# Kernel optimization log

Hardware: AMD Instinct MI355X
Metric: run time of the kernel (lower is better)

Reference implementation:

```python
import jax, jax.numpy as jnp
import numpy as np
import math

DIM = 512
HEADS = 8
DH = DIM // HEADS
B, C, H, W = 2, 512, 48, 48


def setup_inputs() -> dict:
    key = jax.random.key(0)
    k1, k2, k3, k4 = jax.random.split(key, 4)
    x = jax.random.normal(k1, (B, C, H, W), dtype=jnp.float32)
    # torch Linear weights: [out_features, in_features]
    w_qkv = jax.random.normal(k2, (3 * DIM, DIM), dtype=jnp.float32) * (DIM ** -0.5)
    w_out = jax.random.normal(k3, (DIM, DIM), dtype=jnp.float32) * (DIM ** -0.5)
    b_out = jax.random.normal(k4, (DIM,), dtype=jnp.float32) * 0.01
    wavelength = jnp.asarray(0.1, dtype=jnp.float32)
    return {"x": x, "w_qkv": w_qkv, "w_out": w_out, "b_out": b_out, "wavelength": wavelength}


def reference(x, w_qkv, w_out, b_out, wavelength):
    b, c, h, w = x.shape
    n = h * w
    scale = DH ** -0.5

    x_flat = x.reshape(b, c, n).transpose(0, 2, 1)  # [B, N, C]
    qkv = jnp.einsum('bnc,dc->bnd', x_flat, w_qkv)   # [B, N, 3*DIM]
    q, k, v = jnp.split(qkv, 3, axis=-1)

    def to_heads(t):
        return t.reshape(b, n, HEADS, DH).transpose(0, 2, 1, 3)  # [B, h, N, dh]

    q, k, v = to_heads(q), to_heads(k), to_heads(v)

    dots = jnp.einsum('bhid,bhjd->bhij', q, k) * scale  # [B, h, N, N]

    # Fresnel interference bias over spatial positions
    yy, xx = jnp.meshgrid(jnp.arange(h), jnp.arange(w), indexing='ij')
    positions = jnp.stack([yy, xx], axis=-1).astype(jnp.float32).reshape(-1, 2)  # [N, 2]
    pos_diff = positions[None, :, :] - positions[:, None, :]  # [N, N, 2]
    distances = jnp.sqrt(jnp.sum(pos_diff ** 2, axis=-1) + 1e-8)  # [N, N]
    phase = 2.0 * math.pi * distances / (jnp.abs(wavelength) * h + 1e-6)
    interference = jnp.cos(phase)

    dots = dots + interference[None, None, :, :] * 0.1
    attn = jax.nn.softmax(dots, axis=-1)
    out = jnp.einsum('bhij,bhjd->bhid', attn, v)  # [B, h, N, dh]
    out = out.transpose(0, 2, 1, 3).reshape(b, n, HEADS * DH)  # [B, N, DIM]
    out = jnp.einsum('bnd,od->bno', out, w_out) + b_out
    return out.transpose(0, 2, 1).reshape(b, c, h, w)
```

## Files before the change

### kernel.cpp

```cpp
#include <hip/hip_runtime.h>
#include <math.h>

#define BB 2
#define CC 512
#define NN 2304
#define NH 8
#define DD 512
#define D3 1536
#define WIDTH 48
#define C1 0.18033688f

typedef _Float16 h8 __attribute__((ext_vector_type(8)));
typedef _Float16 h4 __attribute__((ext_vector_type(4)));
typedef _Float16 h2 __attribute__((ext_vector_type(2)));
typedef float f4 __attribute__((ext_vector_type(4)));

__device__ __forceinline__ void gload16(const void* g, void* s) {
  __builtin_amdgcn_global_load_lds(
      (const __attribute__((address_space(1))) unsigned int*)g,
      (__attribute__((address_space(3))) unsigned int*)s, 16, 0, 0);
}

__global__ __launch_bounds__(128) void btf_k(const float* __restrict__ wavp,
                                             _Float16* __restrict__ btf)
{
  const int t = threadIdx.x;
  const int qbk = blockIdx.x, ktk = blockIdx.y;
  const int w = t >> 6, quad = (t >> 4) & 3, l15 = t & 15;
  const float pc = 6.283185307179586f / (fabsf(wavp[0]) * (float)WIDTH + 1e-6f);
  _Float16* o = btf + (((size_t)qbk * 36 + ktk) * 128 + t) * 32;
#pragma unroll
  for (int g = 0; g < 4; ++g) {
    h8 v;
#pragma unroll
    for (int e = 0; e < 8; ++e) {
      const int j = g * 8 + e;
      const int nt = j >> 4, mt = (j >> 2) & 3, r = j & 3;
      const int q = qbk * 64 + w * 32 + nt * 16 + l15;
      const int k = ktk * 64 + mt * 16 + quad * 4 + r;
      const float dy = (float)(q / WIDTH) - (float)(k / WIDTH);
      const float dx = (float)(q % WIDTH) - (float)(k % WIDTH);
      const float dist = sqrtf(dy * dy + dx * dx + 1e-8f);
      v[e] = (_Float16)(0.1f * __cosf(dist * pc) * 1.44269504f);
    }
    *(h8*)(o + g * 8) = v;
  }
}

__global__ __launch_bounds__(256) void tx_k(const float* __restrict__ x,
                                            _Float16* __restrict__ xt)
{
  __shared__ float Ls[32][33];
  const int t = threadIdx.x;
  const int n0 = blockIdx.x * 32, c0 = blockIdx.y * 32, b = blockIdx.z;
#pragma unroll
  for (int p = 0; p < 4; ++p) {
    const int cl = (t >> 5) + p * 8, nl = t & 31;
    Ls[cl][nl] = x[((size_t)b * CC + c0 + cl) * NN + n0 + nl];
  }
  __syncthreads();
#pragma unroll
  for (int p = 0; p < 2; ++p) {
    const int nl = (t >> 4) + p * 16, cl = (t & 15) * 2;
    h2 v = {(_Float16)Ls[cl][nl], (_Float16)Ls[cl + 1][nl]};
    *(h2*)(xt + ((size_t)b * NN + n0 + nl) * CC + c0 + cl) = v;
  }
}

__global__ __launch_bounds__(256) void convw_k(const float* __restrict__ wq,
                                               const float* __restrict__ wo,
                                               _Float16* __restrict__ wqh,
                                               _Float16* __restrict__ woh)
{
  const int idx = blockIdx.x * 256 + threadIdx.x;
  const int NQ = (D3 * CC) / 4;
  if (idx < NQ) {
    float4 v = *(const float4*)(wq + (size_t)idx * 4);
    h4 o = {(_Float16)v.x, (_Float16)v.y, (_Float16)v.z, (_Float16)v.w};
    *(h4*)(wqh + (size_t)idx * 4) = o;
  } else {
    const int j = idx - NQ;
    float4 v = *(const float4*)(wo + (size_t)j * 4);
    h4 o = {(_Float16)v.x, (_Float16)v.y, (_Float16)v.z, (_Float16)v.w};
    *(h4*)(woh + (size_t)j * 4) = o;
  }
}

__global__ __launch_bounds__(256) void qkv_gemm_k(
    const _Float16* __restrict__ xt, const _Float16* __restrict__ wqh,
    _Float16* __restrict__ qb, _Float16* __restrict__ kb,
    _Float16* __restrict__ vb)
{
  __shared__ _Float16 Xs[128][32];
  __shared__ _Float16 Ws[128][32];
  const int t = threadIdx.x;
  const int lane = t & 63, w = t >> 6;
  const int l15 = lane & 15, quad = lane >> 4;
  const int wm = w & 1, wn = w >> 1;
  const int n0 = blockIdx.x * 128;
  const int d0 = blockIdx.y * 128;
  const int b  = blockIdx.z;
  const bool isv = (d0 >= 2 * DD);
  const _Float16* xb = xt + (size_t)b * NN * CC;

  const int srow = lane >> 2, scol = (lane & 3) * 8;

  f4 acc[4][4];
#pragma unroll
  for (int mt = 0; mt < 4; ++mt)
#pragma unroll
    for (int nt = 0; nt < 4; ++nt) acc[mt][nt] = (f4)(0.f);

  for (int c0 = 0; c0 < CC; c0 += 32) {
#pragma unroll
    for (int r = 0; r < 2; ++r) {
      const int ci = w + r * 4;
      const int row = ci * 16 + srow;
      gload16(xb + (size_t)(n0 + row) * CC + c0 + scol, &Xs[0][0] + ci * 512);
      gload16(wqh + (size_t)(d0 + row) * CC + c0 + scol, &Ws[0][0] + ci * 512);
    }
    __syncthreads();

    h8 wfr[4], xfr[4];
#pragma unroll
    for (int mt = 0; mt < 4; ++mt)
      wfr[mt] = *(const h8*)&Ws[wm * 64 + mt * 16 + l15][quad * 8];
#pragma unroll
    for (int nt = 0; nt < 4; ++nt)
      xfr[nt] = *(const h8*)&Xs[wn * 64 + nt * 16 + l15][quad * 8];

    if (!isv) {
#pragma unroll
      for (int mt = 0; mt < 4; ++mt)
#pragma unroll
        for (int nt = 0; nt < 4; ++nt)
          acc[mt][nt] = __builtin_amdgcn_mfma_f32_16x16x32_f16(
              wfr[mt], xfr[nt], acc[mt][nt], 0, 0, 0);
    } else {
#pragma unroll
      for (int mt = 0; mt < 4; ++mt)
#pragma unroll
        for (int nt = 0; nt < 4; ++nt)
          acc[mt][nt] = __builtin_amdgcn_mfma_f32_16x16x32_f16(
              xfr[nt], wfr[mt], acc[mt][nt], 0, 0, 0);
    }
    __syncthreads();
  }

  if (!isv) {
    const int which = d0 >> 9;
    _Float16* buf = which == 0 ? qb : kb;
    const int h = ((d0 & 511) >> 6) + wm;
#pragma unroll
    for (int mt = 0; mt < 4; ++mt) {
      const int dh = mt * 16 + quad * 4;
#pragma unroll
      for (int nt = 0; nt < 4; ++nt) {
        const int token = n0 + wn * 64 + nt * 16 + l15;
        h4 o = {(_Float16)acc[mt][nt][0], (_Float16)acc[mt][nt][1],
                (_Float16)acc[mt][nt][2], (_Float16)acc[mt][nt][3]};
        *(h4*)(buf + (((size_t)b * NH + h) * NN + token) * 64 + dh) = o;
      }
    }
  } else {
    const int h = ((d0 - 2 * DD) >> 6) + wm;
#pragma unroll
    for (int mt = 0; mt < 4; ++mt) {
      const int dh = mt * 16 + l15;
#pragma unroll
      for (int nt = 0; nt < 4; ++nt) {
        const int token = n0 + wn * 64 + nt * 16 + quad * 4;
        h4 o = {(_Float16)acc[mt][nt][0], (_Float16)acc[mt][nt][1],
                (_Float16)acc[mt][nt][2], (_Float16)acc[mt][nt][3]};
        *(h4*)(vb + (((size_t)b * NH + h) * 64 + dh) * NN + token) = o;
      }
    }
  }
}

__global__ __launch_bounds__(128, 3) void attn_k(
    const _Float16* __restrict__ qb, const _Float16* __restrict__ kb,
    const _Float16* __restrict__ vb, const _Float16* __restrict__ btf,
    _Float16* __restrict__ op, float* __restrict__ lp)
{
  __shared__ _Float16 Ks[64][72];
  __shared__ _Float16 Vs[64][72];
  __shared__ _Float16 Ps[64][72];

  const int t    = threadIdx.x;
  const int lane = t & 63;
  const int w    = t >> 6;
  const int l15  = lane & 15;
  const int quad = lane >> 4;
  const int qtile = blockIdx.x >> 1;
  const int khalf = blockIdx.x & 1;
  const int n0 = qtile * 64;
  const int h  = blockIdx.y;
  const int b  = blockIdx.z;
  const size_t base = ((size_t)b * NH + h) * NN * 64;
  const _Float16* qp = qb + base;
  const _Float16* kp = kb + base;
  const _Float16* vp = vb + base;

  h8 qf[2][2];
#pragma unroll
  for (int nt = 0; nt < 2; ++nt)
#pragma unroll
    for (int ks = 0; ks < 2; ++ks)
      qf[nt][ks] = *(const h8*)(qp + (size_t)(n0 + w * 32 + nt * 16 + l15) * 64 +
                                ks * 32 + quad * 8);

  f4 oc[4][2];
#pragma unroll
  for (int mt = 0; mt < 4; ++mt)
#pragma unroll
    for (int nt = 0; nt < 2; ++nt) oc[mt][nt] = (f4)(0.f);
  float lacc[2][4] = {};

  const _Float16* bp = btf + (((size_t)qtile * 36 + khalf * 18) * 128 + t) * 32;

  for (int kt = 0; kt < 18; ++kt) {
    const int k0 = (khalf * 18 + kt) * 64;
    h8 kr[4], vr[4], bfr[4];
#pragma unroll
    for (int r = 0; r < 4; ++r) {
      const int c = t + r * 128;
      const int row = c >> 3, off = (c & 7) * 8;
      kr[r] = *(const h8*)(kp + (size_t)(k0 + row) * 64 + off);
      vr[r] = *(const h8*)(vp + (size_t)row * NN + k0 + off);
      bfr[r] = *(const h8*)(bp + r * 8);
    }
    bp += 128 * 32;
    __syncthreads();
#pragma unroll
    for (int r = 0; r < 4; ++r) {
      const int c = t + r * 128;
      const int row = c >> 3, off = (c & 7) * 8;
      *(h8*)&Ks[row][off] = kr[r];
      *(h8*)&Vs[row][off] = vr[r];
    }
    __syncthreads();

    f4 st[4][2];
#pragma unroll
    for (int mt = 0; mt < 4; ++mt)
#pragma unroll
      for (int nt = 0; nt < 2; ++nt) st[mt][nt] = (f4)(0.f);
#pragma unroll
    for (int ks = 0; ks < 2; ++ks) {
#pragma unroll
      for (int mt = 0; mt < 4; ++mt) {
        h8 kf = *(const h8*)&Ks[mt * 16 + l15][ks * 32 + quad * 8];
#pragma unroll
        for (int nt = 0; nt < 2; ++nt)
          st[mt][nt] = __builtin_amdgcn_mfma_f32_16x16x32_f16(
              kf, qf[nt][ks], st[mt][nt], 0, 0, 0);
      }
    }

#pragma unroll
    for (int nt = 0; nt < 2; ++nt) {
      const int q = w * 32 + nt * 16 + l15;
#pragma unroll
      for (int mt = 0; mt < 4; ++mt) {
        h4 pk;
#pragma unroll
        for (int r = 0; r < 4; ++r) {
          const int j = nt * 16 + mt * 4 + r;
          const float bias = (float)bfr[j >> 3][j & 7];
          const float p = __builtin_exp2f(st[mt][nt][r] * C1 + bias);
          lacc[nt][r] += p;
          pk[r] = (_Float16)p;
        }
        *(h4*)&Ps[q][mt * 16 + quad * 4] = pk;
      }
    }

#pragma unroll
    for (int ks = 0; ks < 2; ++ks) {
      h8 pf[2];
#pragma unroll
      for (int nt = 0; nt < 2; ++nt)
        pf[nt] = *(const h8*)&Ps[w * 32 + nt * 16 + l15][ks * 32 + quad * 8];
#pragma unroll
      for (int mt = 0; mt < 4; ++mt) {
        h8 vf = *(const h8*)&Vs[mt * 16 + l15][ks * 32 + quad * 8];
#pragma unroll
        for (int nt = 0; nt < 2; ++nt)
          oc[mt][nt] = __builtin_amdgcn_mfma_f32_16x16x32_f16(
              vf, pf[nt], oc[mt][nt], 0, 0, 0);
      }
    }
  }

#pragma unroll
  for (int nt = 0; nt < 2; ++nt) {
    float l = lacc[nt][0] + lacc[nt][1] + lacc[nt][2] + lacc[nt][3];
    l += __shfl_xor(l, 16);
    l += __shfl_xor(l, 32);
    const float inv = 1.f / l;
    const int qi = n0 + w * 32 + nt * 16 + l15;
    _Float16* od = op + (size_t)khalf * BB * NN * DD +
                   ((size_t)b * NN + qi) * DD + h * 64;
#pragma unroll
    for (int mt = 0; mt < 4; ++mt) {
      const int dh = mt * 16 + quad * 4;
      h4 o = {(_Float16)(oc[mt][nt][0] * inv), (_Float16)(oc[mt][nt][1] * inv),
              (_Float16)(oc[mt][nt][2] * inv), (_Float16)(oc[mt][nt][3] * inv)};
      *(h4*)(od + dh) = o;
    }
    if (quad == 0)
      lp[(size_t)khalf * BB * NH * NN + ((size_t)b * NH + h) * NN + qi] = l;
  }
}

__global__ __launch_bounds__(256) void comb_k(
    const _Float16* __restrict__ op, const float* __restrict__ lp,
    _Float16* __restrict__ ho)
{
  const int idx = blockIdx.x * 256 + threadIdx.x;
  const int d8 = idx & 63;
  const int bn = idx >> 6;
  const int n = bn % NN, b = bn / NN;
  const int h = d8 >> 3;
  const float l0 = lp[((size_t)b * NH + h) * NN + n];
  const float l1 = lp[(size_t)BB * NH * NN + ((size_t)b * NH + h) * NN + n];
  const float inv = 1.f / (l0 + l1);
  const float w0 = l0 * inv, w1 = l1 * inv;
  h8 o0 = *(const h8*)(op + (size_t)bn * DD + d8 * 8);
  h8 o1 = *(const h8*)(op + (size_t)BB * NN * DD + (size_t)bn * DD + d8 * 8);
  h8 r;
#pragma unroll
  for (int i = 0; i < 8; ++i)
    r[i] = (_Float16)((float)o0[i] * w0 + (float)o1[i] * w1);
  *(h8*)(ho + (size_t)bn * DD + d8 * 8) = r;
}

__global__ __launch_bounds__(64) void out_gemm_k(
    const _Float16* __restrict__ ho, const _Float16* __restrict__ woh,
    const float* __restrict__ bias, float* __restrict__ out)
{
  __shared__ _Float16 Hs[64][32];
  __shared__ _Float16 Ws2[64][32];
  const int t = threadIdx.x;
  const int l15 = t & 15, quad = t >> 4;
  const int n0 = blockIdx.x * 64;
  const int o0 = blockIdx.y * 64;
  const int b  = blockIdx.z;
  const int srow = t >> 2, scol = (t & 3) * 8;

  f4 acc[4][4];
#pragma unroll
  for (int mt = 0; mt < 4; ++mt)
#pragma unroll
    for (int nt = 0; nt < 4; ++nt) acc[mt][nt] = (f4)(0.f);

  for (int c0 = 0; c0 < DD; c0 += 32) {
#pragma unroll
    for (int ci = 0; ci < 4; ++ci) {
      const int row = ci * 16 + srow;
      gload16(ho + ((size_t)b * NN + n0 + row) * DD + c0 + scol,
              &Hs[0][0] + ci * 512);
      gload16(woh + (size_t)(o0 + row) * DD + c0 + scol,
              &Ws2[0][0] + ci * 512);
    }
    __syncthreads();
    h8 hf[4], wf[4];
#pragma unroll
    for (int mt = 0; mt < 4; ++mt)
      hf[mt] = *(const h8*)&Hs[mt * 16 + l15][quad * 8];
#pragma unroll
    for (int nt = 0; nt < 4; ++nt)
      wf[nt] = *(const h8*)&Ws2[nt * 16 + l15][quad * 8];
#pragma unroll
    for (int mt = 0; mt < 4; ++mt)
#pragma unroll
      for (int nt = 0; nt < 4; ++nt)
        acc[mt][nt] = __builtin_amdgcn_mfma_f32_16x16x32_f16(
            hf[mt], wf[nt], acc[mt][nt], 0, 0, 0);
    __syncthreads();
  }

#pragma unroll
  for (int nt = 0; nt < 4; ++nt) {
    const int o = o0 + nt * 16 + l15;
    const float bv = bias[o];
#pragma unroll
    for (int mt = 0; mt < 4; ++mt) {
      const int token = n0 + mt * 16 + quad * 4;
      float4 v = {acc[mt][nt][0] + bv, acc[mt][nt][1] + bv,
                  acc[mt][nt][2] + bv, acc[mt][nt][3] + bv};
      *(float4*)(out + ((size_t)b * DD + o) * NN + token) = v;
    }
  }
}

extern "C" void kernel_launch(void* const* d_in, const int* in_sizes, int n_in,
                              void* d_out, int out_size, void* d_ws, size_t ws_size,
                              hipStream_t stream)
{
  (void)in_sizes; (void)n_in; (void)out_size; (void)ws_size;
  const float* x     = (const float*)d_in[0];
  const float* w_qkv = (const float*)d_in[1];
  const float* w_out = (const float*)d_in[2];
  const float* b_out = (const float*)d_in[3];
  const float* wav   = (const float*)d_in[4];
  float* out = (float*)d_out;

  const size_t SZ  = (size_t)BB * NH * NN * 64;
  const size_t BTF = (size_t)36 * 36 * 128 * 32;

  _Float16* qb  = (_Float16*)d_ws;
  _Float16* kb  = qb + SZ;
  _Float16* vb  = kb + SZ;
  _Float16* btf = vb + SZ;
  _Float16* op  = btf + BTF;
  float*    lpf = (float*)(op + 2 * SZ);
  _Float16* woh = (_Float16*)(lpf + 2 * (size_t)BB * NH * NN);
  _Float16* ho  = btf;
  _Float16* xt  = op;
  _Float16* wqh = op + SZ;

  btf_k     <<<dim3(36, 36), 128, 0, stream>>>(wav, btf);
  tx_k      <<<dim3(NN / 32, CC / 32, BB), 256, 0, stream>>>(x, xt);
  convw_k   <<<dim3((D3 * CC + DD * DD) / 1024), 256, 0, stream>>>(w_qkv, w_out, wqh, woh);
  qkv_gemm_k<<<dim3(NN / 128, D3 / 128, BB), 256, 0, stream>>>(xt, wqh, qb, kb, vb);
  attn_k    <<<dim3(NN / 64 * 2, NH, BB), 128, 0, stream>>>(qb, kb, vb, btf, op, lpf);
  comb_k    <<<dim3((BB * NN * 64) / 256), 256, 0, stream>>>(op, lpf, ho);
  out_gemm_k<<<dim3(NN / 64, DD / 64, BB), 64, 0, stream>>>(ho, woh, b_out, out);
}
```

Before: 169.3 us.

## Load MFMA operands directly from global memory, dropping shared-memory staging

```diff
diff --git a/kernel.cpp b/kernel.cpp
--- a/kernel.cpp
+++ b/kernel.cpp
@@ -14,12 +14,6 @@
 typedef _Float16 h4 __attribute__((ext_vector_type(4)));
 typedef _Float16 h2 __attribute__((ext_vector_type(2)));
 typedef float f4 __attribute__((ext_vector_type(4)));
-
-__device__ __forceinline__ void gload16(const void* g, void* s) {
-  __builtin_amdgcn_global_load_lds(
-      (const __attribute__((address_space(1))) unsigned int*)g,
-      (__attribute__((address_space(3))) unsigned int*)s, 16, 0, 0);
-}
 
 __global__ __launch_bounds__(128) void btf_k(const float* __restrict__ wavp,
                                              _Float16* __restrict__ btf)
@@ -91,8 +85,6 @@
     _Float16* __restrict__ qb, _Float16* __restrict__ kb,
     _Float16* __restrict__ vb)
 {
-  __shared__ _Float16 Xs[128][32];
-  __shared__ _Float16 Ws[128][32];
   const int t = threadIdx.x;
   const int lane = t & 63, w = t >> 6;
   const int l15 = lane & 15, quad = lane >> 4;
@@ -102,8 +94,8 @@
   const int b  = blockIdx.z;
   const bool isv = (d0 >= 2 * DD);
   const _Float16* xb = xt + (size_t)b * NN * CC;
-
-  const int srow = lane >> 2, scol = (lane & 3) * 8;
+  const _Float16* wp = wqh + (size_t)(d0 + wm * 64 + l15) * CC + quad * 8;
+  const _Float16* xp = xb + (size_t)(n0 + wn * 64 + l15) * CC + quad * 8;
 
   f4 acc[4][4];
 #pragma unroll
@@ -111,24 +103,15 @@
 #pragma unroll
     for (int nt = 0; nt < 4; ++nt) acc[mt][nt] = (f4)(0.f);
 
+#pragma unroll 2
   for (int c0 = 0; c0 < CC; c0 += 32) {
-#pragma unroll
-    for (int r = 0; r < 2; ++r) {
-      const int ci = w + r * 4;
-      const int row = ci * 16 + srow;
-      gload16(xb + (size_t)(n0 + row) * CC + c0 + scol, &Xs[0][0] + ci * 512);
-      gload16(wqh + (size_t)(d0 + row) * CC + c0 + scol, &Ws[0][0] + ci * 512);
-    }
-    __syncthreads();
-
     h8 wfr[4], xfr[4];
 #pragma unroll
     for (int mt = 0; mt < 4; ++mt)
-      wfr[mt] = *(const h8*)&Ws[wm * 64 + mt * 16 + l15][quad * 8];
+      wfr[mt] = *(const h8*)(wp + (size_t)mt * 16 * CC + c0);
 #pragma unroll
     for (int nt = 0; nt < 4; ++nt)
-      xfr[nt] = *(const h8*)&Xs[wn * 64 + nt * 16 + l15][quad * 8];
-
+      xfr[nt] = *(const h8*)(xp + (size_t)nt * 16 * CC + c0);
     if (!isv) {
 #pragma unroll
       for (int mt = 0; mt < 4; ++mt)
@@ -144,7 +127,6 @@
           acc[mt][nt] = __builtin_amdgcn_mfma_f32_16x16x32_f16(
               xfr[nt], wfr[mt], acc[mt][nt], 0, 0, 0);
     }
-    __syncthreads();
   }
 
   if (!isv) {
@@ -183,20 +165,14 @@
     const _Float16* __restrict__ vb, const _Float16* __restrict__ btf,
     _Float16* __restrict__ op, float* __restrict__ lp)
 {
-  __shared__ _Float16 Ks[64][72];
-  __shared__ _Float16 Vs[64][72];
-  __shared__ _Float16 Ps[64][72];
-
-  const int t    = threadIdx.x;
-  const int lane = t & 63;
-  const int w    = t >> 6;
-  const int l15  = lane & 15;
-  const int quad = lane >> 4;
-  const int qtile = blockIdx.x >> 1;
-  const int khalf = blockIdx.x & 1;
-  const int n0 = qtile * 64;
-  const int h  = blockIdx.y;
-  const int b  = blockIdx.z;
+  __shared__ _Float16 Ps[2][32][72];
+  const int t = threadIdx.x;
+  const int lane = t & 63, w = t >> 6;
+  const int l15 = lane & 15, quad = lane >> 4;
+  const int qt = blockIdx.x >> 1;
+  const int s  = blockIdx.x & 1;
+  const int h = blockIdx.y, b = blockIdx.z;
+  const int n0 = qt * 64 + w * 32;
   const size_t base = ((size_t)b * NH + h) * NN * 64;
   const _Float16* qp = qb + base;
   const _Float16* kp = kb + base;
@@ -207,7 +183,7 @@
   for (int nt = 0; nt < 2; ++nt)
 #pragma unroll
     for (int ks = 0; ks < 2; ++ks)
-      qf[nt][ks] = *(const h8*)(qp + (size_t)(n0 + w * 32 + nt * 16 + l15) * 64 +
+      qf[nt][ks] = *(const h8*)(qp + (size_t)(n0 + nt * 16 + l15) * 64 +
                                 ks * 32 + quad * 8);
 
   f4 oc[4][2];
@@ -217,29 +193,21 @@
     for (int nt = 0; nt < 2; ++nt) oc[mt][nt] = (f4)(0.f);
   float lacc[2][4] = {};
 
-  const _Float16* bp = btf + (((size_t)qtile * 36 + khalf * 18) * 128 + t) * 32;
+  const _Float16* bp = btf + (((size_t)qt * 36 + s * 18) * 128 + t) * 32;
 
   for (int kt = 0; kt < 18; ++kt) {
-    const int k0 = (khalf * 18 + kt) * 64;
-    h8 kr[4], vr[4], bfr[4];
-#pragma unroll
-    for (int r = 0; r < 4; ++r) {
-      const int c = t + r * 128;
-      const int row = c >> 3, off = (c & 7) * 8;
-      kr[r] = *(const h8*)(kp + (size_t)(k0 + row) * 64 + off);
-      vr[r] = *(const h8*)(vp + (size_t)row * NN + k0 + off);
-      bfr[r] = *(const h8*)(bp + r * 8);
-    }
+    const int k0 = (s * 18 + kt) * 64;
+    h8 bfr[4];
+#pragma unroll
+    for (int r = 0; r < 4; ++r) bfr[r] = *(const h8*)(bp + r * 8);
     bp += 128 * 32;
-    __syncthreads();
-#pragma unroll
-    for (int r = 0; r < 4; ++r) {
-      const int c = t + r * 128;
-      const int row = c >> 3, off = (c & 7) * 8;
-      *(h8*)&Ks[row][off] = kr[r];
-      *(h8*)&Vs[row][off] = vr[r];
-    }
-    __syncthreads();
+    h8 kf[2][4];
+#pragma unroll
+    for (int ks = 0; ks < 2; ++ks)
+#pragma unroll
+      for (int mt = 0; mt < 4; ++mt)
+        kf[ks][mt] = *(const h8*)(kp + (size_t)(k0 + mt * 16 + l15) * 64 +
+                                  ks * 32 + quad * 8);
 
     f4 st[4][2];
 #pragma unroll
@@ -247,20 +215,25 @@
 #pragma unroll
       for (int nt = 0; nt < 2; ++nt) st[mt][nt] = (f4)(0.f);
 #pragma unroll
-    for (int ks = 0; ks < 2; ++ks) {
-#pragma unroll
-      for (int mt = 0; mt < 4; ++mt) {
-        h8 kf = *(const h8*)&Ks[mt * 16 + l15][ks * 32 + quad * 8];
+    for (int ks = 0; ks < 2; ++ks)
+#pragma unroll
+      for (int mt = 0; mt < 4; ++mt)
 #pragma unroll
         for (int nt = 0; nt < 2; ++nt)
           st[mt][nt] = __builtin_amdgcn_mfma_f32_16x16x32_f16(
-              kf, qf[nt][ks], st[mt][nt], 0, 0, 0);
-      }
-    }
+              kf[ks][mt], qf[nt][ks], st[mt][nt], 0, 0, 0);
+
+    h8 vf[2][4];
+#pragma unroll
+    for (int ks = 0; ks < 2; ++ks)
+#pragma unroll
+      for (int mt = 0; mt < 4; ++mt)
+        vf[ks][mt] = *(const h8*)(vp + (size_t)(mt * 16 + l15) * NN + k0 +
+                                  ks * 32 + quad * 8);
 
 #pragma unroll
     for (int nt = 0; nt < 2; ++nt) {
-      const int q = w * 32 + nt * 16 + l15;
+      const int q = nt * 16 + l15;
 #pragma unroll
       for (int mt = 0; mt < 4; ++mt) {
         h4 pk;
@@ -272,7 +245,7 @@
           lacc[nt][r] += p;
           pk[r] = (_Float16)p;
         }
-        *(h4*)&Ps[q][mt * 16 + quad * 4] = pk;
+        *(h4*)&Ps[w][q][mt * 16 + quad * 4] = pk;
       }
     }
 
@@ -281,15 +254,13 @@
       h8 pf[2];
 #pragma unroll
       for (int nt = 0; nt < 2; ++nt)
-        pf[nt] = *(const h8*)&Ps[w * 32 + nt * 16 + l15][ks * 32 + quad * 8];
-#pragma unroll
-      for (int mt = 0; mt < 4; ++mt) {
-        h8 vf = *(const h8*)&Vs[mt * 16 + l15][ks * 32 + quad * 8];
+        pf[nt] = *(const h8*)&Ps[w][nt * 16 + l15][ks * 32 + quad * 8];
+#pragma unroll
+      for (int mt = 0; mt < 4; ++mt)
 #pragma unroll
         for (int nt = 0; nt < 2; ++nt)
           oc[mt][nt] = __builtin_amdgcn_mfma_f32_16x16x32_f16(
-              vf, pf[nt], oc[mt][nt], 0, 0, 0);
-      }
+              vf[ks][mt], pf[nt], oc[mt][nt], 0, 0, 0);
     }
   }
 
@@ -299,8 +270,8 @@
     l += __shfl_xor(l, 16);
     l += __shfl_xor(l, 32);
     const float inv = 1.f / l;
-    const int qi = n0 + w * 32 + nt * 16 + l15;
-    _Float16* od = op + (size_t)khalf * BB * NN * DD +
+    const int qi = n0 + nt * 16 + l15;
+    _Float16* od = op + (size_t)s * BB * NN * DD +
                    ((size_t)b * NN + qi) * DD + h * 64;
 #pragma unroll
     for (int mt = 0; mt < 4; ++mt) {
@@ -310,7 +281,7 @@
       *(h4*)(od + dh) = o;
     }
     if (quad == 0)
-      lp[(size_t)khalf * BB * NH * NN + ((size_t)b * NH + h) * NN + qi] = l;
+      lp[(size_t)s * BB * NH * NN + ((size_t)b * NH + h) * NN + qi] = l;
   }
 }
 
@@ -340,14 +311,13 @@
     const _Float16* __restrict__ ho, const _Float16* __restrict__ woh,
     const float* __restrict__ bias, float* __restrict__ out)
 {
-  __shared__ _Float16 Hs[64][32];
-  __shared__ _Float16 Ws2[64][32];
   const int t = threadIdx.x;
   const int l15 = t & 15, quad = t >> 4;
   const int n0 = blockIdx.x * 64;
   const int o0 = blockIdx.y * 64;
   const int b  = blockIdx.z;
-  const int srow = t >> 2, scol = (t & 3) * 8;
+  const _Float16* hp = ho + ((size_t)b * NN + n0 + l15) * DD + quad * 8;
+  const _Float16* wp = woh + (size_t)(o0 + l15) * DD + quad * 8;
 
   f4 acc[4][4];
 #pragma unroll
@@ -355,30 +325,21 @@
 #pragma unroll
     for (int nt = 0; nt < 4; ++nt) acc[mt][nt] = (f4)(0.f);
 
+#pragma unroll 2
   for (int c0 = 0; c0 < DD; c0 += 32) {
-#pragma unroll
-    for (int ci = 0; ci < 4; ++ci) {
-      const int row = ci * 16 + srow;
-      gload16(ho + ((size_t)b * NN + n0 + row) * DD + c0 + scol,
-              &Hs[0][0] + ci * 512);
-      gload16(woh + (size_t)(o0 + row) * DD + c0 + scol,
-              &Ws2[0][0] + ci * 512);
-    }
-    __syncthreads();
     h8 hf[4], wf[4];
 #pragma unroll
     for (int mt = 0; mt < 4; ++mt)
-      hf[mt] = *(const h8*)&Hs[mt * 16 + l15][quad * 8];
+      hf[mt] = *(const h8*)(hp + (size_t)mt * 16 * DD + c0);
 #pragma unroll
     for (int nt = 0; nt < 4; ++nt)
-      wf[nt] = *(const h8*)&Ws2[nt * 16 + l15][quad * 8];
+      wf[nt] = *(const h8*)(wp + (size_t)nt * 16 * DD + c0);
 #pragma unroll
     for (int mt = 0; mt < 4; ++mt)
 #pragma unroll
       for (int nt = 0; nt < 4; ++nt)
         acc[mt][nt] = __builtin_amdgcn_mfma_f32_16x16x32_f16(
             hf[mt], wf[nt], acc[mt][nt], 0, 0, 0);
-    __syncthreads();
   }
 
 #pragma unroll
```

New measurement: 231.0 us. 36.5% more time.

## Double-buffer GEMM tiles and prefetch next K/V tile in attention

Applied to the files above, without the earlier changes.

```diff
diff --git a/kernel.cpp b/kernel.cpp
--- a/kernel.cpp
+++ b/kernel.cpp
@@ -86,24 +86,21 @@
   }
 }
 
-__global__ __launch_bounds__(256) void qkv_gemm_k(
+__global__ __launch_bounds__(64) void qkv_gemm_k(
     const _Float16* __restrict__ xt, const _Float16* __restrict__ wqh,
     _Float16* __restrict__ qb, _Float16* __restrict__ kb,
     _Float16* __restrict__ vb)
 {
-  __shared__ _Float16 Xs[128][32];
-  __shared__ _Float16 Ws[128][32];
+  __shared__ _Float16 Xs[2][64][32];
+  __shared__ _Float16 Ws[2][64][32];
   const int t = threadIdx.x;
-  const int lane = t & 63, w = t >> 6;
-  const int l15 = lane & 15, quad = lane >> 4;
-  const int wm = w & 1, wn = w >> 1;
-  const int n0 = blockIdx.x * 128;
-  const int d0 = blockIdx.y * 128;
+  const int l15 = t & 15, quad = t >> 4;
+  const int n0 = blockIdx.x * 64;
+  const int d0 = blockIdx.y * 64;
   const int b  = blockIdx.z;
   const bool isv = (d0 >= 2 * DD);
   const _Float16* xb = xt + (size_t)b * NN * CC;
-
-  const int srow = lane >> 2, scol = (lane & 3) * 8;
+  const int srow = t >> 2, scol = (t & 3) * 8;
 
   f4 acc[4][4];
 #pragma unroll
@@ -111,24 +108,29 @@
 #pragma unroll
     for (int nt = 0; nt < 4; ++nt) acc[mt][nt] = (f4)(0.f);
 
-  for (int c0 = 0; c0 < CC; c0 += 32) {
-#pragma unroll
-    for (int r = 0; r < 2; ++r) {
-      const int ci = w + r * 4;
+  auto stage = [&](int bf, int c0) {
+#pragma unroll
+    for (int ci = 0; ci < 4; ++ci) {
       const int row = ci * 16 + srow;
-      gload16(xb + (size_t)(n0 + row) * CC + c0 + scol, &Xs[0][0] + ci * 512);
-      gload16(wqh + (size_t)(d0 + row) * CC + c0 + scol, &Ws[0][0] + ci * 512);
-    }
+      gload16(xb + (size_t)(n0 + row) * CC + c0 + scol,
+              &Xs[bf][0][0] + ci * 512);
+      gload16(wqh + (size_t)(d0 + row) * CC + c0 + scol,
+              &Ws[bf][0][0] + ci * 512);
+    }
+  };
+
+  stage(0, 0);
+  for (int i = 0; i < 16; ++i) {
+    const int cur = i & 1;
     __syncthreads();
-
+    if (i < 15) stage(cur ^ 1, (i + 1) * 32);
     h8 wfr[4], xfr[4];
 #pragma unroll
     for (int mt = 0; mt < 4; ++mt)
-      wfr[mt] = *(const h8*)&Ws[wm * 64 + mt * 16 + l15][quad * 8];
+      wfr[mt] = *(const h8*)&Ws[cur][mt * 16 + l15][quad * 8];
 #pragma unroll
     for (int nt = 0; nt < 4; ++nt)
-      xfr[nt] = *(const h8*)&Xs[wn * 64 + nt * 16 + l15][quad * 8];
-
+      xfr[nt] = *(const h8*)&Xs[cur][nt * 16 + l15][quad * 8];
     if (!isv) {
 #pragma unroll
       for (int mt = 0; mt < 4; ++mt)
@@ -144,32 +146,31 @@
           acc[mt][nt] = __builtin_amdgcn_mfma_f32_16x16x32_f16(
               xfr[nt], wfr[mt], acc[mt][nt], 0, 0, 0);
     }
-    __syncthreads();
   }
 
   if (!isv) {
     const int which = d0 >> 9;
     _Float16* buf = which == 0 ? qb : kb;
-    const int h = ((d0 & 511) >> 6) + wm;
+    const int h = (d0 & 511) >> 6;
 #pragma unroll
     for (int mt = 0; mt < 4; ++mt) {
       const int dh = mt * 16 + quad * 4;
 #pragma unroll
       for (int nt = 0; nt < 4; ++nt) {
-        const int token = n0 + wn * 64 + nt * 16 + l15;
+        const int token = n0 + nt * 16 + l15;
         h4 o = {(_Float16)acc[mt][nt][0], (_Float16)acc[mt][nt][1],
                 (_Float16)acc[mt][nt][2], (_Float16)acc[mt][nt][3]};
         *(h4*)(buf + (((size_t)b * NH + h) * NN + token) * 64 + dh) = o;
       }
     }
   } else {
-    const int h = ((d0 - 2 * DD) >> 6) + wm;
+    const int h = (d0 - 2 * DD) >> 6;
 #pragma unroll
     for (int mt = 0; mt < 4; ++mt) {
       const int dh = mt * 16 + l15;
 #pragma unroll
       for (int nt = 0; nt < 4; ++nt) {
-        const int token = n0 + wn * 64 + nt * 16 + quad * 4;
+        const int token = n0 + nt * 16 + quad * 4;
         h4 o = {(_Float16)acc[mt][nt][0], (_Float16)acc[mt][nt][1],
                 (_Float16)acc[mt][nt][2], (_Float16)acc[mt][nt][3]};
         *(h4*)(vb + (((size_t)b * NH + h) * 64 + dh) * NN + token) = o;
@@ -185,18 +186,17 @@
 {
   __shared__ _Float16 Ks[64][72];
   __shared__ _Float16 Vs[64][72];
-  __shared__ _Float16 Ps[64][72];
+  __shared__ _Float16 Ps[2][32][72];
 
   const int t    = threadIdx.x;
   const int lane = t & 63;
   const int w    = t >> 6;
   const int l15  = lane & 15;
   const int quad = lane >> 4;
-  const int qtile = blockIdx.x >> 1;
-  const int khalf = blockIdx.x & 1;
-  const int n0 = qtile * 64;
-  const int h  = blockIdx.y;
-  const int b  = blockIdx.z;
+  const int qt = blockIdx.x >> 1;
+  const int s  = blockIdx.x & 1;
+  const int h = blockIdx.y, b = blockIdx.z;
+  const int n0 = qt * 64;
   const size_t base = ((size_t)b * NH + h) * NN * 64;
   const _Float16* qp = qb + base;
   const _Float16* kp = kb + base;
@@ -217,29 +217,45 @@
     for (int nt = 0; nt < 2; ++nt) oc[mt][nt] = (f4)(0.f);
   float lacc[2][4] = {};
 
-  const _Float16* bp = btf + (((size_t)qtile * 36 + khalf * 18) * 128 + t) * 32;
+  const int srow = t >> 3, soff = (t & 7) * 8;
+  const _Float16* bp = btf + (((size_t)qt * 36 + s * 18) * 128 + t) * 32;
+
+  h8 kr[4], vr[4], br[4];
+  {
+    const int k0 = s * 18 * 64;
+#pragma unroll
+    for (int r = 0; r < 4; ++r) {
+      const int row = srow + r * 16;
+      kr[r] = *(const h8*)(kp + (size_t)(k0 + row) * 64 + soff);
+      vr[r] = *(const h8*)(vp + (size_t)row * NN + k0 + soff);
+      br[r] = *(const h8*)(bp + r * 8);
+    }
+  }
 
   for (int kt = 0; kt < 18; ++kt) {
-    const int k0 = (khalf * 18 + kt) * 64;
-    h8 kr[4], vr[4], bfr[4];
+    __syncthreads();
 #pragma unroll
     for (int r = 0; r < 4; ++r) {
-      const int c = t + r * 128;
-      const int row = c >> 3, off = (c & 7) * 8;
-      kr[r] = *(const h8*)(kp + (size_t)(k0 + row) * 64 + off);
-      vr[r] = *(const h8*)(vp + (size_t)row * NN + k0 + off);
-      bfr[r] = *(const h8*)(bp + r * 8);
-    }
-    bp += 128 * 32;
+      const int row = srow + r * 16;
+      *(h8*)&Ks[row][soff] = kr[r];
+      *(h8*)&Vs[row][soff] = vr[r];
+    }
+    h8 bfr[4];
+#pragma unroll
+    for (int r = 0; r < 4; ++r) bfr[r] = br[r];
     __syncthreads();
-#pragma unroll
-    for (int r = 0; r < 4; ++r) {
-      const int c = t + r * 128;
-      const int row = c >> 3, off = (c & 7) * 8;
-      *(h8*)&Ks[row][off] = kr[r];
-      *(h8*)&Vs[row][off] = vr[r];
-    }
-    __syncthreads();
+
+    if (kt < 17) {
+      const int k0n = (s * 18 + kt + 1) * 64;
+      bp += 128 * 32;
+#pragma unroll
+      for (int r = 0; r < 4; ++r) {
+        const int row = srow + r * 16;
+        kr[r] = *(const h8*)(kp + (size_t)(k0n + row) * 64 + soff);
+        vr[r] = *(const h8*)(vp + (size_t)row * NN + k0n + soff);
+        br[r] = *(const h8*)(bp + r * 8);
+      }
+    }
 
     f4 st[4][2];
 #pragma unroll
@@ -247,7 +263,7 @@
 #pragma unroll
       for (int nt = 0; nt < 2; ++nt) st[mt][nt] = (f4)(0.f);
 #pragma unroll
-    for (int ks = 0; ks < 2; ++ks) {
+    for (int ks = 0; ks < 2; ++ks)
 #pragma unroll
       for (int mt = 0; mt < 4; ++mt) {
         h8 kf = *(const h8*)&Ks[mt * 16 + l15][ks * 32 + quad * 8];
@@ -256,11 +272,10 @@
           st[mt][nt] = __builtin_amdgcn_mfma_f32_16x16x32_f16(
               kf, qf[nt][ks], st[mt][nt], 0, 0, 0);
       }
-    }
 
 #pragma unroll
     for (int nt = 0; nt < 2; ++nt) {
-      const int q = w * 32 + nt * 16 + l15;
+      const int q = nt * 16 + l15;
 #pragma unroll
       for (int mt = 0; mt < 4; ++mt) {
         h4 pk;
@@ -272,7 +287,7 @@
           lacc[nt][r] += p;
           pk[r] = (_Float16)p;
         }
-        *(h4*)&Ps[q][mt * 16 + quad * 4] = pk;
+        *(h4*)&Ps[w][q][mt * 16 + quad * 4] = pk;
       }
     }
 
@@ -281,7 +296,7 @@
       h8 pf[2];
 #pragma unroll
       for (int nt = 0; nt < 2; ++nt)
-        pf[nt] = *(const h8*)&Ps[w * 32 + nt * 16 + l15][ks * 32 + quad * 8];
+        pf[nt] = *(const h8*)&Ps[w][nt * 16 + l15][ks * 32 + quad * 8];
 #pragma unroll
       for (int mt = 0; mt < 4; ++mt) {
         h8 vf = *(const h8*)&Vs[mt * 16 + l15][ks * 32 + quad * 8];
@@ -300,7 +315,7 @@
     l += __shfl_xor(l, 32);
     const float inv = 1.f / l;
     const int qi = n0 + w * 32 + nt * 16 + l15;
-    _Float16* od = op + (size_t)khalf * BB * NN * DD +
+    _Float16* od = op + (size_t)s * BB * NN * DD +
                    ((size_t)b * NN + qi) * DD + h * 64;
 #pragma unroll
     for (int mt = 0; mt < 4; ++mt) {
@@ -310,7 +325,7 @@
       *(h4*)(od + dh) = o;
     }
     if (quad == 0)
-      lp[(size_t)khalf * BB * NH * NN + ((size_t)b * NH + h) * NN + qi] = l;
+      lp[(size_t)s * BB * NH * NN + ((size_t)b * NH + h) * NN + qi] = l;
   }
 }
 
@@ -340,8 +355,8 @@
     const _Float16* __restrict__ ho, const _Float16* __restrict__ woh,
     const float* __restrict__ bias, float* __restrict__ out)
 {
-  __shared__ _Float16 Hs[64][32];
-  __shared__ _Float16 Ws2[64][32];
+  __shared__ _Float16 Hs[2][64][32];
+  __shared__ _Float16 Ws2[2][64][32];
   const int t = threadIdx.x;
   const int l15 = t & 15, quad = t >> 4;
   const int n0 = blockIdx.x * 64;
@@ -355,30 +370,35 @@
 #pragma unroll
     for (int nt = 0; nt < 4; ++nt) acc[mt][nt] = (f4)(0.f);
 
-  for (int c0 = 0; c0 < DD; c0 += 32) {
+  auto stage = [&](int bf, int c0) {
 #pragma unroll
     for (int ci = 0; ci < 4; ++ci) {
       const int row = ci * 16 + srow;
       gload16(ho + ((size_t)b * NN + n0 + row) * DD + c0 + scol,
-              &Hs[0][0] + ci * 512);
+              &Hs[bf][0][0] + ci * 512);
       gload16(woh + (size_t)(o0 + row) * DD + c0 + scol,
-              &Ws2[0][0] + ci * 512);
-    }
+              &Ws2[bf][0][0] + ci * 512);
+    }
+  };
+
+  stage(0, 0);
+  for (int i = 0; i < 16; ++i) {
+    const int cur = i & 1;
     __syncthreads();
+    if (i < 15) stage(cur ^ 1, (i + 1) * 32);
     h8 hf[4], wf[4];
 #pragma unroll
     for (int mt = 0; mt < 4; ++mt)
-      hf[mt] = *(const h8*)&Hs[mt * 16 + l15][quad * 8];
+      hf[mt] = *(const h8*)&Hs[cur][mt * 16 + l15][quad * 8];
 #pragma unroll
     for (int nt = 0; nt < 4; ++nt)
-      wf[nt] = *(const h8*)&Ws2[nt * 16 + l15][quad * 8];
+      wf[nt] = *(const h8*)&Ws2[cur][nt * 16 + l15][quad * 8];
 #pragma unroll
     for (int mt = 0; mt < 4; ++mt)
 #pragma unroll
       for (int nt = 0; nt < 4; ++nt)
         acc[mt][nt] = __builtin_amdgcn_mfma_f32_16x16x32_f16(
             hf[mt], wf[nt], acc[mt][nt], 0, 0, 0);
-    __syncthreads();
   }
 
 #pragma unroll
@@ -424,7 +444,7 @@
   btf_k     <<<dim3(36, 36), 128, 0, stream>>>(wav, btf);
   tx_k      <<<dim3(NN / 32, CC / 32, BB), 256, 0, stream>>>(x, xt);
   convw_k   <<<dim3((D3 * CC + DD * DD) / 1024), 256, 0, stream>>>(w_qkv, w_out, wqh, woh);
-  qkv_gemm_k<<<dim3(NN / 128, D3 / 128, BB), 256, 0, stream>>>(xt, wqh, qb, kb, vb);
+  qkv_gemm_k<<<dim3(NN / 64, D3 / 64, BB), 64, 0, stream>>>(xt, wqh, qb, kb, vb);
   attn_k    <<<dim3(NN / 64 * 2, NH, BB), 128, 0, stream>>>(qb, kb, vb, btf, op, lpf);
   comb_k    <<<dim3((BB * NN * 64) / 256), 256, 0, stream>>>(op, lpf, ho);
   out_gemm_k<<<dim3(NN / 64, DD / 64, BB), 64, 0, stream>>>(ho, woh, b_out, out);
```

Result: slower. 177.1 us (+4.6%).
